# Performance work log

Hardware: AMD Instinct MI355X
Metric: run time of the kernel (lower is better)

The kernel has to match this reference:

```python
import jax, jax.numpy as jnp
import numpy as np

NEG = -1e7  # matches -10000000.0 in the original


def _mas_single(x, t_len, m_len):
    """Monotonic alignment search for one sample.
    x: [T, M] masked log-probs; t_len, m_len: scalar int32 lengths.
    Returns hard path [T, M] (float, same dtype as x).
    """
    T, M = x.shape
    trange = jnp.arange(T)

    # ---- forward Viterbi DP: Q[t, j] = x[t, j] + max(Q[t, j-1], Q[t-1, j-1]) within band ----
    def dp_step(prev_col, j):
        # prev_col: Q[:, j-1]
        cQ = jnp.where(trange == j, NEG, prev_col)                      # stay (invalid on diagonal)
        shifted = jnp.concatenate([jnp.full((1,), NEG, x.dtype), prev_col[:-1]])
        pQ = jnp.where(trange == 0, jnp.where(j == 0, 0.0, NEG), shifted)  # advance
        q = x[:, j] + jnp.maximum(cQ, pQ)
        # valid band: max(0, t_len + j - m_len) <= t < min(t_len, j + 1)
        valid = (trange <= j) & (trange >= t_len - m_len + j) & (trange < t_len) & (j < m_len)
        col = jnp.where(valid, q, NEG)
        return col, col

    _, Q = jax.lax.scan(dp_step, jnp.full((T,), NEG, x.dtype), jnp.arange(M))
    Q = Q.T  # [T, M]

    # ---- backtrack: walk from (t_len-1, m_len-1) down to column 0 ----
    def bt_step(t, j):
        active = j < m_len
        col = jnp.where(active, jax.nn.one_hot(t, T, dtype=x.dtype), jnp.zeros((T,), x.dtype))
        jm1 = jnp.maximum(j - 1, 0)
        tm1 = jnp.maximum(t - 1, 0)
        # decrement token if on diagonal or 'advance' path scored higher
        dec = (t == j) | (Q[t, jm1] < Q[tm1, jm1])
        t_new = jnp.where(active & dec, jnp.maximum(t - 1, 0), t)
        return t_new, col

    _, cols = jax.lax.scan(bt_step, t_len - 1, jnp.arange(M - 1, -1, -1))
    return cols[::-1].T  # [T, M]


def setup_inputs() -> dict:
    key = jax.random.key(0)
    k1, _ = jax.random.split(key)
    B, T, M = 32, 384, 1536
    log_p = jax.random.normal(k1, (B, T, M), dtype=jnp.float32)
    mask = jnp.ones((B, T, M), dtype=jnp.float32)
    return {"log_p": log_p, "mask": mask}


def reference(log_p, mask):
    x = log_p * mask
    token_lengths = mask.sum(axis=1)[:, 0].astype(jnp.int32)  # [B]
    mel_lengths = mask.sum(axis=2)[:, 0].astype(jnp.int32)    # [B]
    return jax.vmap(_mas_single)(x, token_lengths, mel_lengths)
```

## Files before the change

### kernel.cpp

```cpp
#include <hip/hip_runtime.h>
#include <cstdint>
#include <cstddef>

constexpr int BB  = 32;
constexpr int TT  = 384;
constexpr int MM  = 1536;
constexpr int W32 = MM / 32;
constexpr int RPT = 6;
constexpr float NEGV = -1.0e7f;

constexpr size_t WS_BITS_SZ = (size_t)BB * W32 * TT * 4;
constexpr size_t WS_A_OFF   = WS_BITS_SZ;

__global__ __launch_bounds__(64) void mas_dp_bt(
    const float* __restrict__ log_p, const float* __restrict__ mk0,
    uint32_t* __restrict__ bits, int* __restrict__ A)
{
  const int b = blockIdx.x;
  const int k = threadIdx.x;
  const float* lp = log_p + (size_t)b * TT * MM;
  const float* mk = mk0  + (size_t)b * TT * MM;
  uint32_t* bitsS = bits + (size_t)b * W32 * TT;
  int* Ab = A + b * 512;

  float ts = 0.f, ms = 0.f;
  for (int t = k; t < TT; t += 64) ts += mk[(size_t)t * MM];
  for (int j = k; j < MM; j += 64) ms += mk[j];
#pragma unroll
  for (int off = 32; off >= 1; off >>= 1) {
    ts += __shfl_xor(ts, off);
    ms += __shfl_xor(ms, off);
  }
  const int t_len = (int)ts;
  const int m_len = (int)ms;
  for (int t = k; t <= TT; t += 64) Ab[t] = (t >= t_len) ? m_len : 0;

  const int r0 = RPT * k;
  float    qp[RPT];
  uint32_t bacc[RPT];
  float4   ring[4][RPT];
#pragma unroll
  for (int i = 0; i < RPT; ++i) { qp[i] = NEGV; bacc[i] = 0u; }
#pragma unroll
  for (int g = 0; g < 2; ++g)
#pragma unroll
    for (int i = 0; i < RPT; ++i)
      ring[g][i] = *(const float4*)(lp + (size_t)(r0 + i) * MM + g * 4);

  int j = 0;
  for (int w = 0; w < W32; ++w) {
#pragma unroll
    for (int g8 = 0; g8 < 8; ++g8) {
      {
        int gp = w * 8 + g8 + 2; if (gp > MM / 4 - 1) gp = MM / 4 - 1;
        const int pb = (g8 + 2) & 3;
#pragma unroll
        for (int i = 0; i < RPT; ++i)
          ring[pb][i] = *(const float4*)(lp + (size_t)(r0 + i) * MM + (size_t)gp * 4);
      }
      const int cb = g8 & 3;
#pragma unroll
      for (int u = 0; u < 4; ++u, ++j) {
        const float sh = __shfl_up(qp[RPT - 1], 1);
        const float qlast = (k == 0) ? ((j == 0) ? 0.0f : NEGV) : sh;
        const uint32_t mbit = 1u << (j & 31);
#pragma unroll
        for (int i = RPT - 1; i >= 0; --i) {
          const float stay = qp[i];
          const float adv  = (i == 0) ? qlast : qp[i - 1];
          const float x = (&ring[cb][i].x)[u];
          qp[i] = x + fmaxf(stay, adv);
          if (stay < adv) bacc[i] |= mbit;
        }
      }
    }
#pragma unroll
    for (int i = 0; i < RPT; ++i) { bitsS[w * TT + r0 + i] = bacc[i]; bacc[i] = 0u; }
  }

  asm volatile("s_waitcnt vmcnt(0)" ::: "memory");

  int t = t_len - 1;
  int jj = m_len - 1;
  if (t <= 0 || jj < 1) return;
  int t_top = t;
  int w_cur = jj >> 5;
  uint32_t word;
  { const int row = t_top - k; word = (row >= 0) ? bitsS[w_cur * TT + row] : 0u; }

  for (int guard = 0; guard < 4096; ++guard) {
    const uint32_t cur = __shfl(word, t_top - t);
    const int bpos = jj & 31;
    uint32_t m = cur & ((bpos == 31) ? 0xffffffffu : ((2u << bpos) - 1u));
    if (w_cur == 0) m &= ~1u;
    if (m == 0u) {
      if (w_cur == 0) break;
      --w_cur; jj = (w_cur << 5) | 31;
      t_top = t;
      const int row = t_top - k;
      word = (row >= 0) ? bitsS[w_cur * TT + row] : 0u;
      continue;
    }
    const int p = 31 - __builtin_clz(m);
    jj = (w_cur << 5) | p;
    if (k == 0) Ab[t] = jj;
    --t; --jj;
    if (t <= 0 || jj < 1) break;
    const int wn = jj >> 5;
    if (wn != w_cur || (t_top - t) > 63) {
      w_cur = wn; t_top = t;
      const int row = t_top - k;
      word = (row >= 0) ? bitsS[w_cur * TT + row] : 0u;
    }
  }
}

__global__ __launch_bounds__(256) void mas_fill(
    const int* __restrict__ A, float* __restrict__ out)
{
  const int idx = blockIdx.x * 256 + threadIdx.x;
  const int nj4 = MM / 4;
  const int j4 = (idx % nj4) * 4;
  const int t  = (idx / nj4) % TT;
  const int b  = idx / (nj4 * TT);
  const int a  = A[b * 512 + t];
  const int e  = A[b * 512 + t + 1];
  float4 v;
  v.x = (j4 + 0 >= a && j4 + 0 < e) ? 1.0f : 0.0f;
  v.y = (j4 + 1 >= a && j4 + 1 < e) ? 1.0f : 0.0f;
  v.z = (j4 + 2 >= a && j4 + 2 < e) ? 1.0f : 0.0f;
  v.w = (j4 + 3 >= a && j4 + 3 < e) ? 1.0f : 0.0f;
  reinterpret_cast<float4*>(out)[idx] = v;
}

extern "C" void kernel_launch(void* const* d_in, const int* in_sizes, int n_in,
                              void* d_out, int out_size, void* d_ws, size_t ws_size,
                              hipStream_t stream) {
  const float* log_p = (const float*)d_in[0];
  const float* maskp = (const float*)d_in[1];
  float* out = (float*)d_out;
  uint32_t* bits = (uint32_t*)d_ws;
  int* A = (int*)((char*)d_ws + WS_A_OFF);

  mas_dp_bt<<<BB, 64, 0, stream>>>(log_p, maskp, bits, A);
  mas_fill<<<(BB * TT * (MM / 4)) / 256, 256, 0, stream>>>(A, out);
}
```

Baseline: 431.3 us.

## Transpose log_p into scratch so the DP loop reads contiguous column slices

Adds a tiled shared-memory transpose kernel that writes log_p in [M, T] layout into the output buffer, used as scratch. The serial DP kernel then loads each column's six rows per thread as contiguous float2 pairs with a deeper prefetch ring, replacing per-row float4 loads strided by M. This is meant to make the latency-bound per-column loads coalesced across the wave. The cost is an extra full read and write pass over the 75MB tensor, plus one more kernel launch.

```diff
diff --git a/kernel.cpp b/kernel.cpp
--- a/kernel.cpp
+++ b/kernel.cpp
@@ -12,14 +12,31 @@
 constexpr size_t WS_BITS_SZ = (size_t)BB * W32 * TT * 4;
 constexpr size_t WS_A_OFF   = WS_BITS_SZ;
 
-__global__ __launch_bounds__(64) void mas_dp_bt(
-    const float* __restrict__ log_p, const float* __restrict__ mk0,
+__global__ __launch_bounds__(256) void mas_transpose(
+    const float* __restrict__ in, float* __restrict__ outT)
+{
+  __shared__ float tile[32][33];
+  const int b  = blockIdx.z;
+  const int t0 = blockIdx.y * 32, j0 = blockIdx.x * 32;
+  const int tx = threadIdx.x, ty = threadIdx.y;
+  const float* ip = in  + (size_t)b * TT * MM;
+  float*       op = outT + (size_t)b * TT * MM;
+#pragma unroll
+  for (int i = 0; i < 4; ++i)
+    tile[ty + 8 * i][tx] = ip[(size_t)(t0 + ty + 8 * i) * MM + j0 + tx];
+  __syncthreads();
+#pragma unroll
+  for (int i = 0; i < 4; ++i)
+    op[(size_t)(j0 + ty + 8 * i) * TT + t0 + tx] = tile[tx][ty + 8 * i];
+}
+
+__global__ __launch_bounds__(64, 1) void mas_main(
+    const float* __restrict__ Tq, const float* __restrict__ mk0,
     uint32_t* __restrict__ bits, int* __restrict__ A)
 {
   const int b = blockIdx.x;
   const int k = threadIdx.x;
-  const float* lp = log_p + (size_t)b * TT * MM;
-  const float* mk = mk0  + (size_t)b * TT * MM;
+  const float* mk = mk0 + (size_t)b * TT * MM;
   uint32_t* bitsS = bits + (size_t)b * W32 * TT;
   int* Ab = A + b * 512;
 
@@ -36,42 +53,46 @@
   for (int t = k; t <= TT; t += 64) Ab[t] = (t >= t_len) ? m_len : 0;
 
   const int r0 = RPT * k;
+  const float* Tp = Tq + (size_t)b * TT * MM;
   float    qp[RPT];
   uint32_t bacc[RPT];
-  float4   ring[4][RPT];
+  float2   rg[8][3];
 #pragma unroll
   for (int i = 0; i < RPT; ++i) { qp[i] = NEGV; bacc[i] = 0u; }
 #pragma unroll
-  for (int g = 0; g < 2; ++g)
-#pragma unroll
-    for (int i = 0; i < RPT; ++i)
-      ring[g][i] = *(const float4*)(lp + (size_t)(r0 + i) * MM + g * 4);
-
-  int j = 0;
+  for (int u = 0; u < 6; ++u) {
+    const float* p = Tp + (size_t)u * TT + r0;
+    rg[u][0] = *(const float2*)p;
+    rg[u][1] = *(const float2*)(p + 2);
+    rg[u][2] = *(const float2*)(p + 4);
+  }
   for (int w = 0; w < W32; ++w) {
 #pragma unroll
-    for (int g8 = 0; g8 < 8; ++g8) {
+    for (int u = 0; u < 32; ++u) {
+      const int j = w * 32 + u;
       {
-        int gp = w * 8 + g8 + 2; if (gp > MM / 4 - 1) gp = MM / 4 - 1;
-        const int pb = (g8 + 2) & 3;
+        int jp = j + 6; if (jp > MM - 1) jp = MM - 1;
+        const float* p = Tp + (size_t)jp * TT + r0;
+        const int s = (u + 6) & 7;
+        rg[s][0] = *(const float2*)p;
+        rg[s][1] = *(const float2*)(p + 2);
+        rg[s][2] = *(const float2*)(p + 4);
+      }
+      const int cs = u & 7;
+      const float x0 = rg[cs][0].x, x1 = rg[cs][0].y;
+      const float x2 = rg[cs][1].x, x3 = rg[cs][1].y;
+      const float x4 = rg[cs][2].x, x5 = rg[cs][2].y;
+      const float sh = __shfl_up(qp[RPT - 1], 1);
+      const float qlast = (k == 0) ? ((j == 0) ? 0.0f : NEGV) : sh;
+      const uint32_t mbit = 1u << u;
 #pragma unroll
-        for (int i = 0; i < RPT; ++i)
-          ring[pb][i] = *(const float4*)(lp + (size_t)(r0 + i) * MM + (size_t)gp * 4);
-      }
-      const int cb = g8 & 3;
-#pragma unroll
-      for (int u = 0; u < 4; ++u, ++j) {
-        const float sh = __shfl_up(qp[RPT - 1], 1);
-        const float qlast = (k == 0) ? ((j == 0) ? 0.0f : NEGV) : sh;
-        const uint32_t mbit = 1u << (j & 31);
-#pragma unroll
-        for (int i = RPT - 1; i >= 0; --i) {
-          const float stay = qp[i];
-          const float adv  = (i == 0) ? qlast : qp[i - 1];
-          const float x = (&ring[cb][i].x)[u];
-          qp[i] = x + fmaxf(stay, adv);
-          if (stay < adv) bacc[i] |= mbit;
-        }
+      for (int i = RPT - 1; i >= 0; --i) {
+        const float stay = qp[i];
+        const float adv  = (i == 0) ? qlast : qp[i - 1];
+        const float x = (i == 0) ? x0 : (i == 1) ? x1 : (i == 2) ? x2
+                      : (i == 3) ? x3 : (i == 4) ? x4 : x5;
+        qp[i] = x + fmaxf(stay, adv);
+        if (stay < adv) bacc[i] |= mbit;
       }
     }
 #pragma unroll
@@ -141,7 +162,9 @@
   float* out = (float*)d_out;
   uint32_t* bits = (uint32_t*)d_ws;
   int* A = (int*)((char*)d_ws + WS_A_OFF);
+  float* Tq = out;
 
-  mas_dp_bt<<<BB, 64, 0, stream>>>(log_p, maskp, bits, A);
+  mas_transpose<<<dim3(MM / 32, TT / 32, BB), dim3(32, 8), 0, stream>>>(log_p, Tq);
+  mas_main<<<BB, 64, 0, stream>>>(Tq, maskp, bits, A);
   mas_fill<<<(BB * TT * (MM / 4)) / 256, 256, 0, stream>>>(A, out);
 }
```

Measured after the change: 721.0 us. +67.2%, slower.
